# Optimization experiments

Hardware: AMD Instinct MI355X
Metric: run time of the kernel (lower is better)

## Reference

```python
import jax, jax.numpy as jnp
import numpy as np

# Config matching init_kwargs: lat_size=512, fin=64, fout=64, fhidden=128,
# dim=2, kernel_size=1, stride=1, padding=0, groups=1, lat_factor=1.
B, FIN, FOUT, FHID, H, W = 16, 64, 64, 128, 128, 128
LAT = 512
LS = 512            # self.lat_size (lat_size > 3 so unchanged) * lat_factor
HID1 = 1024         # LinearResidualBlock default hidden = fin + fout
HID2 = 1024         # second LRB hidden = self.lat_size * lat_factor * 2
SIZES = [FHID*FIN, FHID*FHID, FOUT*FHID, FOUT*FIN, FHID, FHID, FOUT, FOUT]
KTOT = int(np.sum(SIZES))  # 37248
OFFS = np.cumsum([0] + SIZES)


def setup_inputs() -> dict:
    key = jax.random.key(0)
    ks = jax.random.split(key, 10)
    def w(k, shape):
        return (jax.random.normal(k, shape, jnp.float32) / np.sqrt(shape[0])).astype(jnp.float32)
    return {
        "x": jax.random.normal(ks[0], (B, FIN, H, W), jnp.float32),
        "lat": jax.random.normal(ks[1], (B, LAT), jnpp := jnp.float32) if False else jax.random.normal(ks[1], (B, LAT), jnp.float32),
        # dyna_k = Linear(LAT, LS) -> LRB(LS, LS) -> LRB(LS, KTOT, hidden=HID2)
        "dk_w": w(ks[2], (LAT, LS)), "dk_b": jnp.zeros((LS,), jnp.float32),
        "l1_w1": w(ks[3], (LS, HID1)), "l1_b1": jnp.zeros((HID1,), jnp.float32),
        "l1_w2": w(ks[4], (HID1, LS)), "l1_b2": jnp.zeros((LS,), jnp.float32),
        "l2_w1": w(ks[5], (LS, HID2)), "l2_b1": jnp.zeros((HID2,), jnp.float32),
        "l2_w2": w(ks[6], (HID2, KTOT)), "l2_b2": jnp.zeros((KTOT,), jnp.float32),
        "l2_ws": w(ks[7], (LS, KTOT)),  # shortcut linear (fin != fout)
    }


def _lrb(h, w1, b1, w2, b2, ws=None):
    # LinearResidualBlock: shortcut(h) + Linear(ReLU(Linear(h)))
    sc = h if ws is None else h @ ws
    return sc + jax.nn.relu(h @ w1 + b1) @ w2 + b2


def _hyper(lat, dk_w, dk_b, l1_w1, l1_b1, l1_w2, l1_b2, l2_w1, l2_b1, l2_w2, l2_b2, l2_ws):
    h = lat @ dk_w + dk_b
    h = _lrb(h, l1_w1, l1_b1, l1_w2, l1_b2)          # fin == fout -> identity shortcut
    return _lrb(h, l2_w1, l2_b1, l2_w2, l2_b2, l2_ws)


def _dyna_block(x, ksv):
    # Split hypernet output into per-sample 1x1 conv kernels and biases.
    k_in = ksv[:, OFFS[0]:OFFS[1]].reshape(B, FHID, FIN)
    k_mid = ksv[:, OFFS[1]:OFFS[2]].reshape(B, FHID, FHID)
    k_out = ksv[:, OFFS[2]:OFFS[3]].reshape(B, FOUT, FHID)
    k_sh = ksv[:, OFFS[3]:OFFS[4]].reshape(B, FOUT, FIN)
    b_in = ksv[:, OFFS[4]:OFFS[5]][:, :, None, None]
    b_mid = ksv[:, OFFS[5]:OFFS[6]][:, :, None, None]
    b_out = ksv[:, OFFS[6]:OFFS[7]][:, :, None, None]
    b_sh = ksv[:, OFFS[7]:OFFS[8]][:, :, None, None]
    # groups = batch trick == per-sample 1x1 conv == batched channel GEMM
    xs = jnp.einsum('boi,bihw->bohw', k_sh, x) + b_sh
    hh = jax.nn.relu(jnp.einsum('boi,bihw->bohw', k_in, x) + b_in)
    hh = jax.nn.relu(jnp.einsum('boi,bihw->bohw', k_mid, hh) + b_mid)
    return jnp.einsum('boi,bihw->bohw', k_out, hh) + b_out + xs


def reference(x, lat, dk_w, dk_b, l1_w1, l1_b1, l1_w2, l1_b2, l2_w1, l2_b1, l2_w2, l2_b2, l2_ws):
    ksv = _hyper(lat, dk_w, dk_b, l1_w1, l1_b1, l1_w2, l1_b2, l2_w1, l2_b1, l2_w2, l2_b2, l2_ws)
    return _dyna_block(x, ksv)  # [B, FOUT, H, W]
```

## Files before the change

kernel.cpp:

```cpp
#include <hip/hip_runtime.h>

#define N_KSV 37248
#define N_KW  36864

typedef float f32x4 __attribute__((ext_vector_type(4)));
typedef short short8 __attribute__((ext_vector_type(8)));
typedef short short4v __attribute__((ext_vector_type(4)));
typedef __bf16 bf16x8 __attribute__((ext_vector_type(8)));

__device__ inline short f2bs(float f) {
  unsigned u = __builtin_bit_cast(unsigned, f);
  u += 0x7fffu + ((u >> 16) & 1u);
  return (short)(u >> 16);
}

__device__ inline f32x4 mfma16(short8 a, short8 b, f32x4 c) {
  return __builtin_amdgcn_mfma_f32_16x16x32_bf16(
      __builtin_bit_cast(bf16x8, a), __builtin_bit_cast(bf16x8, b), c, 0, 0, 0);
}

__global__ void k_h0(const float* __restrict__ lat, const float* __restrict__ w,
                     const float* __restrict__ bias, float* __restrict__ h0) {
  int j = blockIdx.x * 256 + threadIdx.x;
  int b = blockIdx.y;
  const float* lp = lat + b * 512;
  float acc = bias[j];
#pragma unroll 16
  for (int k = 0; k < 512; ++k) acc = fmaf(lp[k], w[k * 512 + j], acc);
  h0[b * 512 + j] = acc;
}

__global__ void k_t1(const float* __restrict__ h0, const float* __restrict__ w,
                     const float* __restrict__ bias, float* __restrict__ t1) {
  int j = blockIdx.x * 256 + threadIdx.x;
  int b = blockIdx.y;
  const float* hp = h0 + b * 512;
  float acc = bias[j];
#pragma unroll 16
  for (int k = 0; k < 512; ++k) acc = fmaf(hp[k], w[k * 1024 + j], acc);
  t1[b * 1024 + j] = fmaxf(acc, 0.f);
}

__global__ void k_h(const float* __restrict__ h0, const float* __restrict__ t1,
                    const float* __restrict__ w, const float* __restrict__ bias,
                    float* __restrict__ h, short* __restrict__ hxT) {
  int j = blockIdx.x * 256 + threadIdx.x;
  int b = blockIdx.y;
  const float* tp = t1 + b * 1024;
  float acc = bias[j];
#pragma unroll 16
  for (int k = 0; k < 1024; ++k) acc = fmaf(tp[k], w[k * 512 + j], acc);
  float v = acc + h0[b * 512 + j];
  h[b * 512 + j] = v;
  hxT[b * 1536 + j] = f2bs(v);
}

__global__ void k_t2(const float* __restrict__ h, const float* __restrict__ w,
                     const float* __restrict__ bias, short* __restrict__ hxT) {
  int j = blockIdx.x * 256 + threadIdx.x;
  int b = blockIdx.y;
  const float* hp = h + b * 512;
  float acc = bias[j];
#pragma unroll 16
  for (int k = 0; k < 512; ++k) acc = fmaf(hp[k], w[k * 1024 + j], acc);
  hxT[b * 1536 + 512 + j] = f2bs(fmaxf(acc, 0.f));
}

#define LOADB(dst, ktv) { \
    const float* bp_ = ((ktv) < 16) ? (wsp + (size_t)((ktv) * 32) * N_KSV) \
                                    : (w2p + (size_t)((ktv) * 32 - 512) * N_KSV); \
    dst[0] = *reinterpret_cast<const f32x4*>(bp_); \
    dst[1] = *reinterpret_cast<const f32x4*>(bp_ + (size_t)1 * N_KSV); \
    dst[2] = *reinterpret_cast<const f32x4*>(bp_ + (size_t)2 * N_KSV); \
    dst[3] = *reinterpret_cast<const f32x4*>(bp_ + (size_t)3 * N_KSV); \
    dst[4] = *reinterpret_cast<const f32x4*>(bp_ + (size_t)4 * N_KSV); \
    dst[5] = *reinterpret_cast<const f32x4*>(bp_ + (size_t)5 * N_KSV); \
    dst[6] = *reinterpret_cast<const f32x4*>(bp_ + (size_t)6 * N_KSV); \
    dst[7] = *reinterpret_cast<const f32x4*>(bp_ + (size_t)7 * N_KSV); }

#define LOADA(dst, ktv) \
    dst = *reinterpret_cast<const short8*>(apb + (ktv) * 32);

#define COMPUTE(bsrc, asrc) { \
    _Pragma("unroll") \
    for (int t = 0; t < 4; ++t) { \
      short8 bf_; \
      bf_[0] = f2bs(bsrc[0][t]); bf_[1] = f2bs(bsrc[1][t]); \
      bf_[2] = f2bs(bsrc[2][t]); bf_[3] = f2bs(bsrc[3][t]); \
      bf_[4] = f2bs(bsrc[4][t]); bf_[5] = f2bs(bsrc[5][t]); \
      bf_[6] = f2bs(bsrc[6][t]); bf_[7] = f2bs(bsrc[7][t]); \
      acc[t] = mfma16(asrc, bf_, acc[t]); \
    } }

__global__ __launch_bounds__(256, 4) void k5_mfma(
    const float* __restrict__ wsm, const float* __restrict__ w2,
    const short* __restrict__ hxT, const float* __restrict__ b2,
    float* __restrict__ ksv, short* __restrict__ kwb) {
  __shared__ f32x4 red[3][64][4];
  const int tid = threadIdx.x;
  const int wv = tid >> 6;
  const int lane = tid & 63;
  const int col0 = blockIdx.x * 64;
  const int l15 = lane & 15;
  const int lg = lane >> 4;

  const float* wsp = wsm + (size_t)(lg * 8) * N_KSV + col0 + l15 * 4;
  const float* w2p = w2 + (size_t)(lg * 8) * N_KSV + col0 + l15 * 4;
  const short* apb = hxT + l15 * 1536 + lg * 8;

  f32x4 acc[4];
#pragma unroll
  for (int t = 0; t < 4; ++t) acc[t] = (f32x4){0.f, 0.f, 0.f, 0.f};

  const int kt0 = wv * 12;
  f32x4 bA[8], bB[8];
  short8 aA, aB;
  LOADB(bA, kt0);
  LOADA(aA, kt0);

#pragma unroll
  for (int s = 0; s < 12; ++s) {
    if (s + 1 < 12) {
      if ((s & 1) == 0) {
        LOADB(bB, kt0 + s + 1);
        LOADA(aB, kt0 + s + 1);
      } else {
        LOADB(bA, kt0 + s + 1);
        LOADA(aA, kt0 + s + 1);
      }
    }
    if ((s & 1) == 0) COMPUTE(bA, aA) else COMPUTE(bB, aB)
  }

  if (wv > 0) {
#pragma unroll
    for (int t = 0; t < 4; ++t) red[wv - 1][lane][t] = acc[t];
  }
  __syncthreads();
  if (wv != 0) return;

#pragma unroll
  for (int t = 0; t < 4; ++t) {
    acc[t] += red[0][lane][t];
    acc[t] += red[1][lane][t];
    acc[t] += red[2][lane][t];
  }

  const int m0 = lg * 4;
#pragma unroll
  for (int t = 0; t < 4; ++t) {
    const int col = col0 + l15 * 4 + t;
    const float bias = b2[col];
#pragma unroll
    for (int r = 0; r < 4; ++r) {
      float s = acc[t][r] + bias;
      ksv[(size_t)(m0 + r) * N_KSV + col] = s;
      if (col < N_KW)
        kwb[(size_t)(m0 + r) * N_KW + col] = f2bs(s);
    }
  }
}

__device__ inline int xT_idx(int p, int c) {
  return p * 64 + ((((c >> 3) ^ (p & 7)) << 3) | (c & 7));
}
__device__ inline int h_idx(int p, int c) {
  return p * 128 + ((((c >> 3) ^ (p & 7)) << 3) | (c & 7));
}

__global__ __launch_bounds__(256) void k_dyna(const float* __restrict__ x,
                                              const short* __restrict__ kwb,
                                              const float* __restrict__ ksv,
                                              float* __restrict__ out) {
  __shared__ __align__(16) short lds[20480];
  short* xT = lds;
  short* h1 = lds + 4096;
  short* h2 = lds + 12288;

  const int tid = threadIdx.x;
  const int lane = tid & 63;
  const int w = tid >> 6;
  const int l15 = lane & 15;
  const int lg = lane >> 4;

  const int b = blockIdx.x >> 8;
  const int pos0 = (blockIdx.x & 255) << 6;

  const float* xb = x + ((size_t)b << 20) + pos0;
  const short* kw = kwb + b * N_KW;
  const float* bias = ksv + (size_t)b * N_KSV + N_KW;

#pragma unroll
  for (int i = 0; i < 8; ++i) {
    int p = lane;
    int cp = i * 4 + w;
    int c = cp * 2;
    float v0 = __builtin_nontemporal_load(xb + (size_t)c * 16384 + p);
    float v1 = __builtin_nontemporal_load(xb + (size_t)(c + 1) * 16384 + p);
    int idx = xT_idx(p, c);
    int pk = (int)(unsigned short)f2bs(v0) | ((int)f2bs(v1) << 16);
    *reinterpret_cast<int*>(&xT[idx]) = pk;
  }
  __syncthreads();

  short8 a1[2][2];
#pragma unroll
  for (int mt = 0; mt < 2; ++mt)
#pragma unroll
    for (int kf = 0; kf < 2; ++kf)
      a1[mt][kf] = *reinterpret_cast<const short8*>(
          kw + (w * 32 + mt * 16 + l15) * 64 + kf * 32 + lg * 8);

  f32x4 zero = {0.f, 0.f, 0.f, 0.f};
  f32x4 acc1[2][4];
#pragma unroll
  for (int mt = 0; mt < 2; ++mt)
#pragma unroll
    for (int nt = 0; nt < 4; ++nt) acc1[mt][nt] = zero;

#pragma unroll
  for (int nt = 0; nt < 4; ++nt) {
    int p = nt * 16 + l15;
    short8 b0 = *reinterpret_cast<const short8*>(&xT[xT_idx(p, lg * 8)]);
    short8 b1 = *reinterpret_cast<const short8*>(&xT[xT_idx(p, 32 + lg * 8)]);
#pragma unroll
    for (int mt = 0; mt < 2; ++mt) {
      acc1[mt][nt] = mfma16(a1[mt][0], b0, acc1[mt][nt]);
      acc1[mt][nt] = mfma16(a1[mt][1], b1, acc1[mt][nt]);
    }
  }
#pragma unroll
  for (int mt = 0; mt < 2; ++mt) {
    int ch0 = w * 32 + mt * 16 + lg * 4;
    f32x4 bv = *reinterpret_cast<const f32x4*>(bias + ch0);
#pragma unroll
    for (int nt = 0; nt < 4; ++nt) {
      int p = nt * 16 + l15;
      short4v hv;
#pragma unroll
      for (int jj = 0; jj < 4; ++jj)
        hv[jj] = f2bs(fmaxf(acc1[mt][nt][jj] + bv[jj], 0.f));
      *reinterpret_cast<short4v*>(&h1[h_idx(p, ch0)]) = hv;
    }
  }
  __syncthreads();

  short8 a2[2][4];
#pragma unroll
  for (int mt = 0; mt < 2; ++mt)
#pragma unroll
    for (int kf = 0; kf < 4; ++kf)
      a2[mt][kf] = *reinterpret_cast<const short8*>(
          kw + 8192 + (w * 32 + mt * 16 + l15) * 128 + kf * 32 + lg * 8);

  f32x4 acc2[2][4];
#pragma unroll
  for (int mt = 0; mt < 2; ++mt)
#pragma unroll
    for (int nt = 0; nt < 4; ++nt) acc2[mt][nt] = zero;

#pragma unroll
  for (int nt = 0; nt < 4; ++nt) {
    int p = nt * 16 + l15;
    short8 bb[4];
#pragma unroll
    for (int kf = 0; kf < 4; ++kf)
      bb[kf] = *reinterpret_cast<const short8*>(&h1[h_idx(p, kf * 32 + lg * 8)]);
#pragma unroll
    for (int mt = 0; mt < 2; ++mt)
#pragma unroll
      for (int kf = 0; kf < 4; ++kf)
        acc2[mt][nt] = mfma16(a2[mt][kf], bb[kf], acc2[mt][nt]);
  }
#pragma unroll
  for (int mt = 0; mt < 2; ++mt) {
    int ch0 = w * 32 + mt * 16 + lg * 4;
    f32x4 bv = *reinterpret_cast<const f32x4*>(bias + 128 + ch0);
#pragma unroll
    for (int nt = 0; nt < 4; ++nt) {
      int p = nt * 16 + l15;
      short4v hv;
#pragma unroll
      for (int jj = 0; jj < 4; ++jj)
        hv[jj] = f2bs(fmaxf(acc2[mt][nt][jj] + bv[jj], 0.f));
      *reinterpret_cast<short4v*>(&h2[h_idx(p, ch0)]) = hv;
    }
  }
  __syncthreads();

  short8 a3[4], ash[2];
#pragma unroll
  for (int kf = 0; kf < 4; ++kf)
    a3[kf] = *reinterpret_cast<const short8*>(
        kw + 24576 + (w * 16 + l15) * 128 + kf * 32 + lg * 8);
#pragma unroll
  for (int kf = 0; kf < 2; ++kf)
    ash[kf] = *reinterpret_cast<const short8*>(
        kw + 32768 + (w * 16 + l15) * 64 + kf * 32 + lg * 8);

  int ch0 = w * 16 + lg * 4;
  f32x4 bo = *reinterpret_cast<const f32x4*>(bias + 256 + ch0);
  f32x4 bs = *reinterpret_cast<const f32x4*>(bias + 320 + ch0);

#pragma unroll
  for (int nt = 0; nt < 4; ++nt) {
    int p = nt * 16 + l15;
    f32x4 acc = zero;
#pragma unroll
    for (int kf = 0; kf < 4; ++kf) {
      short8 bb = *reinterpret_cast<const short8*>(&h2[h_idx(p, kf * 32 + lg * 8)]);
      acc = mfma16(a3[kf], bb, acc);
    }
#pragma unroll
    for (int kf = 0; kf < 2; ++kf) {
      short8 bb = *reinterpret_cast<const short8*>(&xT[xT_idx(p, kf * 32 + lg * 8)]);
      acc = mfma16(ash[kf], bb, acc);
    }
#pragma unroll
    for (int jj = 0; jj < 4; ++jj)
      __builtin_nontemporal_store(acc[jj] + bo[jj] + bs[jj],
          out + ((size_t)(b * 64 + ch0 + jj) << 14) + pos0 + p);
  }
}

extern "C" void kernel_launch(void* const* d_in, const int* in_sizes, int n_in,
                              void* d_out, int out_size, void* d_ws, size_t ws_size,
                              hipStream_t stream) {
  const float* x    = (const float*)d_in[0];
  const float* lat  = (const float*)d_in[1];
  const float* dk_w = (const float*)d_in[2];
  const float* dk_b = (const float*)d_in[3];
  const float* l1w1 = (const float*)d_in[4];
  const float* l1b1 = (const float*)d_in[5];
  const float* l1w2 = (const float*)d_in[6];
  const float* l1b2 = (const float*)d_in[7];
  const float* l2w1 = (const float*)d_in[8];
  const float* l2b1 = (const float*)d_in[9];
  const float* l2w2 = (const float*)d_in[10];
  const float* l2b2 = (const float*)d_in[11];
  const float* l2ws = (const float*)d_in[12];
  float* out = (float*)d_out;
  float* wsf = (float*)d_ws;

  float* h0  = wsf;
  float* t1  = wsf + 8192;
  float* h   = wsf + 24576;
  float* ksv = wsf + 32768;
  short* hxT = (short*)(wsf + 628736);
  short* kwb = hxT + 24576;

  k_h0<<<dim3(2, 16), 256, 0, stream>>>(lat, dk_w, dk_b, h0);
  k_t1<<<dim3(4, 16), 256, 0, stream>>>(h0, l1w1, l1b1, t1);
  k_h <<<dim3(2, 16), 256, 0, stream>>>(h0, t1, l1w2, l1b2, h, hxT);
  k_t2<<<dim3(4, 16), 256, 0, stream>>>(h, l2w1, l2b1, hxT);
  k5_mfma<<<dim3(N_KSV / 64), 256, 0, stream>>>(l2ws, l2w2, hxT, l2b2, ksv, kwb);
  k_dyna<<<dim3(4096), 256, 0, stream>>>(x, kwb, ksv, out);
}
```

Measured before the change: 193.0 us.

## Process two pixel tiles per block and prefetch x with vector loads

Each block of the dynamic-conv kernel now handles two 64-pixel tiles instead of one, so the grid is halved. Both tiles' x data are fetched up front with 16-byte nontemporal loads, replacing scalar loads. The second tile is converted into LDS while the first tile's later layers run, overlapping global-load latency with MFMA work. The price is extra LDS for a second x buffer and higher register pressure from holding the prefetched tile, which may lower occupancy.

```diff
diff --git a/kernel.cpp b/kernel.cpp
--- a/kernel.cpp
+++ b/kernel.cpp
@@ -12,6 +12,10 @@
   unsigned u = __builtin_bit_cast(unsigned, f);
   u += 0x7fffu + ((u >> 16) & 1u);
   return (short)(u >> 16);
+}
+
+__device__ inline f32x4 ntl4(const float* p) {
+  return __builtin_nontemporal_load(reinterpret_cast<const f32x4*>(p));
 }
 
 __device__ inline f32x4 mfma16(short8 a, short8 b, f32x4 c) {
@@ -168,14 +172,141 @@
   return p * 128 + ((((c >> 3) ^ (p & 7)) << 3) | (c & 7));
 }
 
+__device__ __forceinline__ void dyna_L1(const short* xT, short* h1s,
+    const short* kw, const float* bias, int w, int l15, int lg) {
+  short8 a1[2][2];
+#pragma unroll
+  for (int mt = 0; mt < 2; ++mt)
+#pragma unroll
+    for (int kf = 0; kf < 2; ++kf)
+      a1[mt][kf] = *reinterpret_cast<const short8*>(
+          kw + (w * 32 + mt * 16 + l15) * 64 + kf * 32 + lg * 8);
+
+  f32x4 acc1[2][4];
+#pragma unroll
+  for (int mt = 0; mt < 2; ++mt)
+#pragma unroll
+    for (int nt = 0; nt < 4; ++nt) acc1[mt][nt] = (f32x4){0.f, 0.f, 0.f, 0.f};
+
+#pragma unroll
+  for (int nt = 0; nt < 4; ++nt) {
+    int p = nt * 16 + l15;
+    short8 b0 = *reinterpret_cast<const short8*>(&xT[xT_idx(p, lg * 8)]);
+    short8 b1 = *reinterpret_cast<const short8*>(&xT[xT_idx(p, 32 + lg * 8)]);
+#pragma unroll
+    for (int mt = 0; mt < 2; ++mt) {
+      acc1[mt][nt] = mfma16(a1[mt][0], b0, acc1[mt][nt]);
+      acc1[mt][nt] = mfma16(a1[mt][1], b1, acc1[mt][nt]);
+    }
+  }
+#pragma unroll
+  for (int mt = 0; mt < 2; ++mt) {
+    int ch0 = w * 32 + mt * 16 + lg * 4;
+    f32x4 bv = *reinterpret_cast<const f32x4*>(bias + ch0);
+#pragma unroll
+    for (int nt = 0; nt < 4; ++nt) {
+      int p = nt * 16 + l15;
+      short4v hv;
+#pragma unroll
+      for (int jj = 0; jj < 4; ++jj)
+        hv[jj] = f2bs(fmaxf(acc1[mt][nt][jj] + bv[jj], 0.f));
+      *reinterpret_cast<short4v*>(&h1s[h_idx(p, ch0)]) = hv;
+    }
+  }
+}
+
+__device__ __forceinline__ void dyna_L2(const short* h1s, short* h2s,
+    const short* kw, const float* bias, int w, int l15, int lg) {
+  short8 a2[2][4];
+#pragma unroll
+  for (int mt = 0; mt < 2; ++mt)
+#pragma unroll
+    for (int kf = 0; kf < 4; ++kf)
+      a2[mt][kf] = *reinterpret_cast<const short8*>(
+          kw + 8192 + (w * 32 + mt * 16 + l15) * 128 + kf * 32 + lg * 8);
+
+  f32x4 acc2[2][4];
+#pragma unroll
+  for (int mt = 0; mt < 2; ++mt)
+#pragma unroll
+    for (int nt = 0; nt < 4; ++nt) acc2[mt][nt] = (f32x4){0.f, 0.f, 0.f, 0.f};
+
+#pragma unroll
+  for (int nt = 0; nt < 4; ++nt) {
+    int p = nt * 16 + l15;
+    short8 bb[4];
+#pragma unroll
+    for (int kf = 0; kf < 4; ++kf)
+      bb[kf] = *reinterpret_cast<const short8*>(&h1s[h_idx(p, kf * 32 + lg * 8)]);
+#pragma unroll
+    for (int mt = 0; mt < 2; ++mt)
+#pragma unroll
+      for (int kf = 0; kf < 4; ++kf)
+        acc2[mt][nt] = mfma16(a2[mt][kf], bb[kf], acc2[mt][nt]);
+  }
+#pragma unroll
+  for (int mt = 0; mt < 2; ++mt) {
+    int ch0 = w * 32 + mt * 16 + lg * 4;
+    f32x4 bv = *reinterpret_cast<const f32x4*>(bias + 128 + ch0);
+#pragma unroll
+    for (int nt = 0; nt < 4; ++nt) {
+      int p = nt * 16 + l15;
+      short4v hv;
+#pragma unroll
+      for (int jj = 0; jj < 4; ++jj)
+        hv[jj] = f2bs(fmaxf(acc2[mt][nt][jj] + bv[jj], 0.f));
+      *reinterpret_cast<short4v*>(&h2s[h_idx(p, ch0)]) = hv;
+    }
+  }
+}
+
+__device__ __forceinline__ void dyna_L3(const short* h2s, const short* xT,
+    const short* kw, const float* bias, float* outb, int pos0,
+    int w, int l15, int lg) {
+  short8 a3[4], ash[2];
+#pragma unroll
+  for (int kf = 0; kf < 4; ++kf)
+    a3[kf] = *reinterpret_cast<const short8*>(
+        kw + 24576 + (w * 16 + l15) * 128 + kf * 32 + lg * 8);
+#pragma unroll
+  for (int kf = 0; kf < 2; ++kf)
+    ash[kf] = *reinterpret_cast<const short8*>(
+        kw + 32768 + (w * 16 + l15) * 64 + kf * 32 + lg * 8);
+
+  int ch0 = w * 16 + lg * 4;
+  f32x4 bo = *reinterpret_cast<const f32x4*>(bias + 256 + ch0);
+  f32x4 bs = *reinterpret_cast<const f32x4*>(bias + 320 + ch0);
+
+#pragma unroll
+  for (int nt = 0; nt < 4; ++nt) {
+    int p = nt * 16 + l15;
+    f32x4 acc = {0.f, 0.f, 0.f, 0.f};
+#pragma unroll
+    for (int kf = 0; kf < 4; ++kf) {
+      short8 bb = *reinterpret_cast<const short8*>(&h2s[h_idx(p, kf * 32 + lg * 8)]);
+      acc = mfma16(a3[kf], bb, acc);
+    }
+#pragma unroll
+    for (int kf = 0; kf < 2; ++kf) {
+      short8 bb = *reinterpret_cast<const short8*>(&xT[xT_idx(p, kf * 32 + lg * 8)]);
+      acc = mfma16(ash[kf], bb, acc);
+    }
+#pragma unroll
+    for (int jj = 0; jj < 4; ++jj)
+      __builtin_nontemporal_store(acc[jj] + bo[jj] + bs[jj],
+          outb + (((size_t)(ch0 + jj)) << 14) + pos0 + p);
+  }
+}
+
 __global__ __launch_bounds__(256) void k_dyna(const float* __restrict__ x,
                                               const short* __restrict__ kwb,
                                               const float* __restrict__ ksv,
                                               float* __restrict__ out) {
-  __shared__ __align__(16) short lds[20480];
-  short* xT = lds;
-  short* h1 = lds + 4096;
-  short* h2 = lds + 12288;
+  __shared__ __align__(16) short lds[24576];
+  short* xTA = lds;
+  short* xTB = lds + 4096;
+  short* h1s = lds + 8192;
+  short* h2s = lds + 16384;
 
   const int tid = threadIdx.x;
   const int lane = tid & 63;
@@ -183,144 +314,48 @@
   const int l15 = lane & 15;
   const int lg = lane >> 4;
 
-  const int b = blockIdx.x >> 8;
-  const int pos0 = (blockIdx.x & 255) << 6;
-
-  const float* xb = x + ((size_t)b << 20) + pos0;
+  const int b = blockIdx.x >> 7;
+  const int pos0A = (blockIdx.x & 127) << 7;
+  const int pos0B = pos0A + 64;
+
+  const float* xb = x + ((size_t)b << 20);
   const short* kw = kwb + b * N_KW;
   const float* bias = ksv + (size_t)b * N_KSV + N_KW;
-
-#pragma unroll
-  for (int i = 0; i < 8; ++i) {
-    int p = lane;
-    int cp = i * 4 + w;
-    int c = cp * 2;
-    float v0 = __builtin_nontemporal_load(xb + (size_t)c * 16384 + p);
-    float v1 = __builtin_nontemporal_load(xb + (size_t)(c + 1) * 16384 + p);
-    int idx = xT_idx(p, c);
-    int pk = (int)(unsigned short)f2bs(v0) | ((int)f2bs(v1) << 16);
-    *reinterpret_cast<int*>(&xT[idx]) = pk;
-  }
-  __syncthreads();
-
-  short8 a1[2][2];
-#pragma unroll
-  for (int mt = 0; mt < 2; ++mt)
-#pragma unroll
-    for (int kf = 0; kf < 2; ++kf)
-      a1[mt][kf] = *reinterpret_cast<const short8*>(
-          kw + (w * 32 + mt * 16 + l15) * 64 + kf * 32 + lg * 8);
-
-  f32x4 zero = {0.f, 0.f, 0.f, 0.f};
-  f32x4 acc1[2][4];
-#pragma unroll
-  for (int mt = 0; mt < 2; ++mt)
-#pragma unroll
-    for (int nt = 0; nt < 4; ++nt) acc1[mt][nt] = zero;
-
-#pragma unroll
-  for (int nt = 0; nt < 4; ++nt) {
-    int p = nt * 16 + l15;
-    short8 b0 = *reinterpret_cast<const short8*>(&xT[xT_idx(p, lg * 8)]);
-    short8 b1 = *reinterpret_cast<const short8*>(&xT[xT_idx(p, 32 + lg * 8)]);
-#pragma unroll
-    for (int mt = 0; mt < 2; ++mt) {
-      acc1[mt][nt] = mfma16(a1[mt][0], b0, acc1[mt][nt]);
-      acc1[mt][nt] = mfma16(a1[mt][1], b1, acc1[mt][nt]);
-    }
-  }
-#pragma unroll
-  for (int mt = 0; mt < 2; ++mt) {
-    int ch0 = w * 32 + mt * 16 + lg * 4;
-    f32x4 bv = *reinterpret_cast<const f32x4*>(bias + ch0);
-#pragma unroll
-    for (int nt = 0; nt < 4; ++nt) {
-      int p = nt * 16 + l15;
-      short4v hv;
-#pragma unroll
-      for (int jj = 0; jj < 4; ++jj)
-        hv[jj] = f2bs(fmaxf(acc1[mt][nt][jj] + bv[jj], 0.f));
-      *reinterpret_cast<short4v*>(&h1[h_idx(p, ch0)]) = hv;
-    }
-  }
-  __syncthreads();
-
-  short8 a2[2][4];
-#pragma unroll
-  for (int mt = 0; mt < 2; ++mt)
-#pragma unroll
-    for (int kf = 0; kf < 4; ++kf)
-      a2[mt][kf] = *reinterpret_cast<const short8*>(
-          kw + 8192 + (w * 32 + mt * 16 + l15) * 128 + kf * 32 + lg * 8);
-
-  f32x4 acc2[2][4];
-#pragma unroll
-  for (int mt = 0; mt < 2; ++mt)
-#pragma unroll
-    for (int nt = 0; nt < 4; ++nt) acc2[mt][nt] = zero;
-
-#pragma unroll
-  for (int nt = 0; nt < 4; ++nt) {
-    int p = nt * 16 + l15;
-    short8 bb[4];
-#pragma unroll
-    for (int kf = 0; kf < 4; ++kf)
-      bb[kf] = *reinterpret_cast<const short8*>(&h1[h_idx(p, kf * 32 + lg * 8)]);
-#pragma unroll
-    for (int mt = 0; mt < 2; ++mt)
-#pragma unroll
-      for (int kf = 0; kf < 4; ++kf)
-        acc2[mt][nt] = mfma16(a2[mt][kf], bb[kf], acc2[mt][nt]);
-  }
-#pragma unroll
-  for (int mt = 0; mt < 2; ++mt) {
-    int ch0 = w * 32 + mt * 16 + lg * 4;
-    f32x4 bv = *reinterpret_cast<const f32x4*>(bias + 128 + ch0);
-#pragma unroll
-    for (int nt = 0; nt < 4; ++nt) {
-      int p = nt * 16 + l15;
-      short4v hv;
-#pragma unroll
-      for (int jj = 0; jj < 4; ++jj)
-        hv[jj] = f2bs(fmaxf(acc2[mt][nt][jj] + bv[jj], 0.f));
-      *reinterpret_cast<short4v*>(&h2[h_idx(p, ch0)]) = hv;
-    }
-  }
-  __syncthreads();
-
-  short8 a3[4], ash[2];
-#pragma unroll
-  for (int kf = 0; kf < 4; ++kf)
-    a3[kf] = *reinterpret_cast<const short8*>(
-        kw + 24576 + (w * 16 + l15) * 128 + kf * 32 + lg * 8);
-#pragma unroll
-  for (int kf = 0; kf < 2; ++kf)
-    ash[kf] = *reinterpret_cast<const short8*>(
-        kw + 32768 + (w * 16 + l15) * 64 + kf * 32 + lg * 8);
-
-  int ch0 = w * 16 + lg * 4;
-  f32x4 bo = *reinterpret_cast<const f32x4*>(bias + 256 + ch0);
-  f32x4 bs = *reinterpret_cast<const f32x4*>(bias + 320 + ch0);
-
-#pragma unroll
-  for (int nt = 0; nt < 4; ++nt) {
-    int p = nt * 16 + l15;
-    f32x4 acc = zero;
-#pragma unroll
-    for (int kf = 0; kf < 4; ++kf) {
-      short8 bb = *reinterpret_cast<const short8*>(&h2[h_idx(p, kf * 32 + lg * 8)]);
-      acc = mfma16(a3[kf], bb, acc);
-    }
-#pragma unroll
-    for (int kf = 0; kf < 2; ++kf) {
-      short8 bb = *reinterpret_cast<const short8*>(&xT[xT_idx(p, kf * 32 + lg * 8)]);
-      acc = mfma16(ash[kf], bb, acc);
-    }
-#pragma unroll
-    for (int jj = 0; jj < 4; ++jj)
-      __builtin_nontemporal_store(acc[jj] + bo[jj] + bs[jj],
-          out + ((size_t)(b * 64 + ch0 + jj) << 14) + pos0 + p);
-  }
+  float* outb = out + ((size_t)b << 20);
+
+  const int cc = (tid >> 3) * 2;
+  const int p0 = (tid & 7) * 8;
+  const float* xrow = xb + (size_t)cc * 16384 + p0;
+
+  f32x4 a0 = ntl4(xrow + pos0A),        a1v = ntl4(xrow + pos0A + 4);
+  f32x4 a2v = ntl4(xrow + 16384 + pos0A), a3v = ntl4(xrow + 16384 + pos0A + 4);
+  f32x4 b0 = ntl4(xrow + pos0B),        b1v = ntl4(xrow + pos0B + 4);
+  f32x4 b2v = ntl4(xrow + 16384 + pos0B), b3v = ntl4(xrow + 16384 + pos0B + 4);
+
+#define WRITEX(xT, r0, r1, r2, r3) { \
+    _Pragma("unroll") \
+    for (int i = 0; i < 8; ++i) { \
+      float va = (i < 4) ? r0[i] : r1[i - 4]; \
+      float vb = (i < 4) ? r2[i] : r3[i - 4]; \
+      int pk = (int)(unsigned short)f2bs(va) | ((int)f2bs(vb) << 16); \
+      *reinterpret_cast<int*>(&(xT)[xT_idx(p0 + i, cc)]) = pk; \
+    } }
+
+  WRITEX(xTA, a0, a1v, a2v, a3v);
+  __syncthreads();
+
+  dyna_L1(xTA, h1s, kw, bias, w, l15, lg);
+  __syncthreads();
+  dyna_L2(h1s, h2s, kw, bias, w, l15, lg);
+  WRITEX(xTB, b0, b1v, b2v, b3v);
+  __syncthreads();
+  dyna_L3(h2s, xTA, kw, bias, outb, pos0A, w, l15, lg);
+  dyna_L1(xTB, h1s, kw, bias, w, l15, lg);
+  __syncthreads();
+  dyna_L2(h1s, h2s, kw, bias, w, l15, lg);
+  __syncthreads();
+  dyna_L3(h2s, xTB, kw, bias, outb, pos0B, w, l15, lg);
+#undef WRITEX
 }
 
 extern "C" void kernel_launch(void* const* d_in, const int* in_sizes, int n_in,
@@ -354,5 +389,5 @@
   k_h <<<dim3(2, 16), 256, 0, stream>>>(h0, t1, l1w2, l1b2, h, hxT);
   k_t2<<<dim3(4, 16), 256, 0, stream>>>(h, l2w1, l2b1, hxT);
   k5_mfma<<<dim3(N_KSV / 64), 256, 0, stream>>>(l2ws, l2w2, hxT, l2b2, ksv, kwb);
-  k_dyna<<<dim3(4096), 256, 0, stream>>>(x, kwb, ksv, out);
-}
+  k_dyna<<<dim3(2048), 256, 0, stream>>>(x, kwb, ksv, out);
+}
```

Measured after the change: 191.7 us. No clear change (-0.7%).
